# Kernel optimization log

Measured on AMD Instinct MI355X. Metric: run time of the kernel, lower is better.

The kernel has to match this reference:

```python
import jax, jax.numpy as jnp
import numpy as np

WINDOW_SIZE = 128  # matches init_kwargs


def setup_inputs() -> dict:
    key = jax.random.key(0)
    kq, kk, kv = jax.random.split(key, 3)
    B, H, S, D = 1, 8, 2048, 64
    q = jax.random.normal(kq, (B, H, S, D), dtype=jnp.float32)
    k = jax.random.normal(kk, (B, H, S, D), dtype=jnp.float32)
    v = jax.random.normal(kv, (B, H, S, D), dtype=jnp.float32)
    return {"q": q, "k": k, "v": v}


def reference(q, k, v):
    # q, k, v: [B, H, S, D]
    B, H, S, D = q.shape
    w = WINDOW_SIZE // 2  # half-window = 64
    offs = jnp.arange(-w, w + 1)                      # [W] with W = 2w+1 = 129
    pos = jnp.arange(S)[:, None] + offs[None, :]      # [S, W] absolute key index per query
    valid = (pos >= 0) & (pos < S)                    # edge clipping: start=max(0,i-w), end=min(S,i+w+1)
    pos_c = jnp.clip(pos, 0, S - 1)

    # Gather banded keys/values: [B, H, S, W, D]
    k_win = k[:, :, pos_c, :]
    v_win = v[:, :, pos_c, :]

    scale = 1.0 / jnp.sqrt(jnp.asarray(D, dtype=q.dtype))
    scores = jnp.einsum('bhsd,bhswd->bhsw', q, k_win) * scale  # [B, H, S, W]
    neg_inf = jnp.asarray(-jnp.inf, dtype=scores.dtype)
    scores = jnp.where(valid[None, None, :, :], scores, neg_inf)

    attn = jax.nn.softmax(scores, axis=-1)            # every row has >= w+1 valid entries, no NaNs
    out = jnp.einsum('bhsw,bhswd->bhsd', attn, v_win) # [B, H, S, D]
    return out
```

## Files before the change

kernel.cpp:

```cpp
#include <hip/hip_runtime.h>
#include <hip/hip_fp16.h>


#define SEQ 2048
#define NH 8
#define QB 64
#define ROWS 192
#define KSTR 72
#define PSTR 40

typedef _Float16 f16x8 __attribute__((ext_vector_type(8)));
typedef float    f32x4 __attribute__((ext_vector_type(4)));

static __device__ __forceinline__ ushort4 pack4(float4 f, float s) {
    union { _Float16 h[4]; ushort4 u; } p;
    p.h[0] = (_Float16)(f.x * s);
    p.h[1] = (_Float16)(f.y * s);
    p.h[2] = (_Float16)(f.z * s);
    p.h[3] = (_Float16)(f.w * s);
    return p.u;
}

__global__ __launch_bounds__(512) void local_attn(
    const float* __restrict__ q,
    const float* __restrict__ k,
    const float* __restrict__ v,
    float* __restrict__ out)
{
    __shared__ __align__(16) _Float16      Kl[ROWS * KSTR];
    __shared__ __align__(16) unsigned char VtB[64 * 384];
    __shared__ __align__(16) _Float16      Pm[8][16 * PSTR];
    __shared__ __align__(16) float         Cmb[4][64][20];

    const int tid  = threadIdx.x;
    const int lane = tid & 63;
    const int w    = tid >> 6;
    const int t    = w & 3;
    const int half = w >> 2;
    const int l15  = lane & 15;
    const int l4   = lane >> 4;
    const int bx   = blockIdx.x;
    const int h     = bx & 7;
    const int qbase = (bx >> 3) * QB;

    const float* kh = k + (size_t)h * SEQ * 64;
    const float* vh = v + (size_t)h * SEQ * 64;
    const float* qh = q + (size_t)h * SEQ * 64;

    const float* qrow = qh + (size_t)(qbase + t * 16 + l15) * 64 + l4 * 8;
    float4 q0 = *(const float4*)(qrow);
    float4 q1 = *(const float4*)(qrow + 4);
    float4 q2 = *(const float4*)(qrow + 32);
    float4 q3 = *(const float4*)(qrow + 36);
    union uf { f16x8 v; _Float16 hh[8]; };
    uf A0, A1;
    A0.hh[0] = (_Float16)(q0.x * 0.125f); A0.hh[1] = (_Float16)(q0.y * 0.125f);
    A0.hh[2] = (_Float16)(q0.z * 0.125f); A0.hh[3] = (_Float16)(q0.w * 0.125f);
    A0.hh[4] = (_Float16)(q1.x * 0.125f); A0.hh[5] = (_Float16)(q1.y * 0.125f);
    A0.hh[6] = (_Float16)(q1.z * 0.125f); A0.hh[7] = (_Float16)(q1.w * 0.125f);
    A1.hh[0] = (_Float16)(q2.x * 0.125f); A1.hh[1] = (_Float16)(q2.y * 0.125f);
    A1.hh[2] = (_Float16)(q2.z * 0.125f); A1.hh[3] = (_Float16)(q2.w * 0.125f);
    A1.hh[4] = (_Float16)(q3.x * 0.125f); A1.hh[5] = (_Float16)(q3.y * 0.125f);
    A1.hh[6] = (_Float16)(q3.z * 0.125f); A1.hh[7] = (_Float16)(q3.w * 0.125f);

    {
        const int d4  = (tid & 15) << 2;
        const int lr0 = tid >> 4;
        #pragma unroll
        for (int it = 0; it < 6; ++it) {
            const int lr = lr0 + it * 32;
            const int g  = qbase - 64 + lr;
            float4 kv4 = make_float4(0.f, 0.f, 0.f, 0.f);
            float4 vv4 = make_float4(0.f, 0.f, 0.f, 0.f);
            if (g >= 0 && g < SEQ) {
                kv4 = *(const float4*)(kh + (size_t)g * 64 + d4);
                vv4 = *(const float4*)(vh + (size_t)g * 64 + d4);
            }
            *(ushort4*)&Kl[lr * KSTR + d4] = pack4(kv4, 1.0f);
            float vs[4] = {vv4.x, vv4.y, vv4.z, vv4.w};
            #pragma unroll
            for (int i2 = 0; i2 < 4; ++i2) {
                int d = d4 + i2;
                int u = (lr >> 3) ^ (d & 7);
                *(_Float16*)&VtB[d * 384 + (u << 4) + (lr & 7) * 2] = (_Float16)vs[i2];
            }
        }
    }
    __syncthreads();

    _Float16* Pw = Pm[w];
    float rsum[4] = {0.f, 0.f, 0.f, 0.f};
    f32x4 o[4];
    #pragma unroll
    for (int dt = 0; dt < 4; ++dt) o[dt] = (f32x4){0.f, 0.f, 0.f, 0.f};

    #pragma unroll
    for (int c = 0; c < 3; ++c) {
        const int r0 = (half * 3 + c) * 32;

        #pragma unroll
        for (int t2 = 0; t2 < 2; ++t2) {
            const int r = r0 + t2 * 16 + l15;
            f16x8 b0 = *(const f16x8*)&Kl[r * KSTR + l4 * 8];
            f16x8 b1 = *(const f16x8*)&Kl[r * KSTR + 32 + l4 * 8];
            f32x4 cacc = {0.f, 0.f, 0.f, 0.f};
            cacc = __builtin_amdgcn_mfma_f32_16x16x32_f16(A0.v, b0, cacc, 0, 0, 0);
            cacc = __builtin_amdgcn_mfma_f32_16x16x32_f16(A1.v, b1, cacc, 0, 0, 0);
            const int g  = qbase - 64 + r;
            const bool gv = (g >= 0) & (g < SEQ);
            #pragma unroll
            for (int j = 0; j < 4; ++j) {
                const int qg = qbase + t * 16 + l4 * 4 + j;
                const bool valid = gv && (g >= qg - 64) && (g <= qg + 64);
                const float e = valid ? __expf(cacc[j]) : 0.f;
                rsum[j] += e;
                Pw[(l4 * 4 + j) * PSTR + t2 * 16 + l15] = (_Float16)e;
            }
        }

        asm volatile("s_waitcnt lgkmcnt(0)" ::: "memory");

        f16x8 a = *(const f16x8*)&Pw[l15 * PSTR + l4 * 8];
        #pragma unroll
        for (int dt = 0; dt < 4; ++dt) {
            const int dim = dt * 16 + l15;
            const int u   = ((r0 + l4 * 8) >> 3) ^ (dim & 7);
            f16x8 bb = *(const f16x8*)&VtB[dim * 384 + (u << 4)];
            o[dt] = __builtin_amdgcn_mfma_f32_16x16x32_f16(a, bb, o[dt], 0, 0, 0);
        }
    }

    if (half == 1) {
        #pragma unroll
        for (int dt = 0; dt < 4; ++dt)
            *(f32x4*)&Cmb[t][lane][dt * 4] = o[dt];
        f32x4 pr = {rsum[0], rsum[1], rsum[2], rsum[3]};
        *(f32x4*)&Cmb[t][lane][16] = pr;
    }
    __syncthreads();
    if (half == 0) {
        #pragma unroll
        for (int dt = 0; dt < 4; ++dt) {
            f32x4 p = *(const f32x4*)&Cmb[t][lane][dt * 4];
            o[dt] += p;
        }
        f32x4 pr = *(const f32x4*)&Cmb[t][lane][16];

        #pragma unroll
        for (int j = 0; j < 4; ++j) {
            float l = rsum[j] + pr[j];
            l += __shfl_xor(l, 1, 64);
            l += __shfl_xor(l, 2, 64);
            l += __shfl_xor(l, 4, 64);
            l += __shfl_xor(l, 8, 64);
            const float inv = 1.0f / l;
            const int qg = qbase + t * 16 + l4 * 4 + j;
            #pragma unroll
            for (int dt = 0; dt < 4; ++dt)
                out[((size_t)h * SEQ + qg) * 64 + dt * 16 + l15] = o[dt][j] * inv;
        }
    }
}

extern "C" void kernel_launch(void* const* d_in, const int* in_sizes, int n_in,
                              void* d_out, int out_size, void* d_ws, size_t ws_size,
                              hipStream_t stream)
{
    const float* q = (const float*)d_in[0];
    const float* k = (const float*)d_in[1];
    const float* v = (const float*)d_in[2];
    float* out = (float*)d_out;

    local_attn<<<256, 512, 0, stream>>>(q, k, v, out);
}
```

Measured before the change: 11.81 us.

## Halve query tile to 32 rows and run 512 blocks of 256 threads

Shrinks each block to 32 queries with a 160-row key/value band and four waves instead of eight. This launches twice as many blocks, so all CUs get work and each block has a shorter prologue. The score/PV chunk loop becomes an explicit 3-versus-2 chunk split between the two wave halves. In exchange, more K/V rows are reloaded per query and the two halves carry uneven work.

```diff
diff --git a/kernel.cpp b/kernel.cpp
--- a/kernel.cpp
+++ b/kernel.cpp
@@ -4,8 +4,8 @@
 
 #define SEQ 2048
 #define NH 8
-#define QB 64
-#define ROWS 192
+#define QB 32
+#define ROWS 160
 #define KSTR 72
 #define PSTR 40
 
@@ -21,7 +21,7 @@
     return p.u;
 }
 
-__global__ __launch_bounds__(512) void local_attn(
+__global__ __launch_bounds__(256, 2) void local_attn(
     const float* __restrict__ q,
     const float* __restrict__ k,
     const float* __restrict__ v,
@@ -29,14 +29,14 @@
 {
     __shared__ __align__(16) _Float16      Kl[ROWS * KSTR];
     __shared__ __align__(16) unsigned char VtB[64 * 384];
-    __shared__ __align__(16) _Float16      Pm[8][16 * PSTR];
-    __shared__ __align__(16) float         Cmb[4][64][20];
+    __shared__ __align__(16) _Float16      Pm[4][16 * PSTR];
+    __shared__ __align__(16) float         Cmb[2][64][20];
 
     const int tid  = threadIdx.x;
     const int lane = tid & 63;
     const int w    = tid >> 6;
-    const int t    = w & 3;
-    const int half = w >> 2;
+    const int t    = w & 1;
+    const int half = w >> 1;
     const int l15  = lane & 15;
     const int l4   = lane >> 4;
     const int bx   = blockIdx.x;
@@ -67,8 +67,8 @@
         const int d4  = (tid & 15) << 2;
         const int lr0 = tid >> 4;
         #pragma unroll
-        for (int it = 0; it < 6; ++it) {
-            const int lr = lr0 + it * 32;
+        for (int it = 0; it < 10; ++it) {
+            const int lr = lr0 + it * 16;
             const int g  = qbase - 64 + lr;
             float4 kv4 = make_float4(0.f, 0.f, 0.f, 0.f);
             float4 vv4 = make_float4(0.f, 0.f, 0.f, 0.f);
@@ -94,41 +94,48 @@
     #pragma unroll
     for (int dt = 0; dt < 4; ++dt) o[dt] = (f32x4){0.f, 0.f, 0.f, 0.f};
 
-    #pragma unroll
-    for (int c = 0; c < 3; ++c) {
-        const int r0 = (half * 3 + c) * 32;
+#define DO_CHUNK(R0)                                                          \
+    {                                                                         \
+        const int r0 = (R0);                                                  \
+        _Pragma("unroll")                                                     \
+        for (int t2 = 0; t2 < 2; ++t2) {                                      \
+            const int r = r0 + t2 * 16 + l15;                                 \
+            f16x8 b0 = *(const f16x8*)&Kl[r * KSTR + l4 * 8];                 \
+            f16x8 b1 = *(const f16x8*)&Kl[r * KSTR + 32 + l4 * 8];            \
+            f32x4 cacc = {0.f, 0.f, 0.f, 0.f};                                \
+            cacc = __builtin_amdgcn_mfma_f32_16x16x32_f16(A0.v, b0, cacc, 0, 0, 0); \
+            cacc = __builtin_amdgcn_mfma_f32_16x16x32_f16(A1.v, b1, cacc, 0, 0, 0); \
+            const int g  = qbase - 64 + r;                                    \
+            const bool gv = (g >= 0) & (g < SEQ);                             \
+            _Pragma("unroll")                                                 \
+            for (int j = 0; j < 4; ++j) {                                     \
+                const int qg = qbase + t * 16 + l4 * 4 + j;                   \
+                const bool valid = gv && (g >= qg - 64) && (g <= qg + 64);    \
+                const float e = valid ? __expf(cacc[j]) : 0.f;                \
+                rsum[j] += e;                                                 \
+                Pw[(l4 * 4 + j) * PSTR + t2 * 16 + l15] = (_Float16)e;        \
+            }                                                                 \
+        }                                                                     \
+        asm volatile("s_waitcnt lgkmcnt(0)" ::: "memory");                    \
+        f16x8 a = *(const f16x8*)&Pw[l15 * PSTR + l4 * 8];                    \
+        _Pragma("unroll")                                                     \
+        for (int dt = 0; dt < 4; ++dt) {                                      \
+            const int dim = dt * 16 + l15;                                    \
+            const int u   = ((r0 + l4 * 8) >> 3) ^ (dim & 7);                 \
+            f16x8 bb = *(const f16x8*)&VtB[dim * 384 + (u << 4)];             \
+            o[dt] = __builtin_amdgcn_mfma_f32_16x16x32_f16(a, bb, o[dt], 0, 0, 0); \
+        }                                                                     \
+    }
 
-        #pragma unroll
-        for (int t2 = 0; t2 < 2; ++t2) {
-            const int r = r0 + t2 * 16 + l15;
-            f16x8 b0 = *(const f16x8*)&Kl[r * KSTR + l4 * 8];
-            f16x8 b1 = *(const f16x8*)&Kl[r * KSTR + 32 + l4 * 8];
-            f32x4 cacc = {0.f, 0.f, 0.f, 0.f};
-            cacc = __builtin_amdgcn_mfma_f32_16x16x32_f16(A0.v, b0, cacc, 0, 0, 0);
-            cacc = __builtin_amdgcn_mfma_f32_16x16x32_f16(A1.v, b1, cacc, 0, 0, 0);
-            const int g  = qbase - 64 + r;
-            const bool gv = (g >= 0) & (g < SEQ);
-            #pragma unroll
-            for (int j = 0; j < 4; ++j) {
-                const int qg = qbase + t * 16 + l4 * 4 + j;
-                const bool valid = gv && (g >= qg - 64) && (g <= qg + 64);
-                const float e = valid ? __expf(cacc[j]) : 0.f;
-                rsum[j] += e;
-                Pw[(l4 * 4 + j) * PSTR + t2 * 16 + l15] = (_Float16)e;
-            }
-        }
-
-        asm volatile("s_waitcnt lgkmcnt(0)" ::: "memory");
-
-        f16x8 a = *(const f16x8*)&Pw[l15 * PSTR + l4 * 8];
-        #pragma unroll
-        for (int dt = 0; dt < 4; ++dt) {
-            const int dim = dt * 16 + l15;
-            const int u   = ((r0 + l4 * 8) >> 3) ^ (dim & 7);
-            f16x8 bb = *(const f16x8*)&VtB[dim * 384 + (u << 4)];
-            o[dt] = __builtin_amdgcn_mfma_f32_16x16x32_f16(a, bb, o[dt], 0, 0, 0);
-        }
+    if (half == 0) {
+        DO_CHUNK(0)
+        DO_CHUNK(32)
+        DO_CHUNK(64)
+    } else {
+        DO_CHUNK(96)
+        DO_CHUNK(128)
     }
+#undef DO_CHUNK
 
     if (half == 1) {
         #pragma unroll
@@ -171,5 +178,5 @@
     const float* v = (const float*)d_in[2];
     float* out = (float*)d_out;
 
-    local_attn<<<256, 512, 0, stream>>>(q, k, v, out);
+    local_attn<<<512, 256, 0, stream>>>(q, k, v, out);
 }
```

Result: slower. 12.79 us (+8.3%).

## Pre-convert K/V to swizzled fp16 workspace and load via global_load_lds

Applied to the files above, without the earlier changes.

Adds a separate pre-pass kernel that converts K and V to fp16 once into a padded, XOR-swizzled workspace, with V stored transposed. The attention kernel then copies its K/V tiles directly into LDS using global_load_lds DMA instead of per-thread float loads, conversion and scattered transposed stores. This removes the repeated conversion of overlapping windows and the bank-conflicted V transpose in the main kernel. In exchange it adds a second kernel launch and an extra workspace write and read, and it falls back to the old kernel when the workspace is too small.

```diff
diff --git a/kernel.cpp b/kernel.cpp
--- a/kernel.cpp
+++ b/kernel.cpp
@@ -6,28 +6,210 @@
 #define NH 8
 #define QB 64
 #define ROWS 192
-#define KSTR 72
 #define PSTR 40
+
+#define KHEAD 278528
+#define VOFF  2228224
+#define VROW  4352
+#define WSNEED (VOFF + 8 * 278528)
 
 typedef _Float16 f16x8 __attribute__((ext_vector_type(8)));
 typedef float    f32x4 __attribute__((ext_vector_type(4)));
 
-static __device__ __forceinline__ ushort4 pack4(float4 f, float s) {
-    union { _Float16 h[4]; ushort4 u; } p;
-    p.h[0] = (_Float16)(f.x * s);
-    p.h[1] = (_Float16)(f.y * s);
-    p.h[2] = (_Float16)(f.z * s);
-    p.h[3] = (_Float16)(f.w * s);
-    return p.u;
+#define GLOAD_LDS16(gsrc, ldst)                                              \
+    __builtin_amdgcn_global_load_lds(                                        \
+        (const __attribute__((address_space(1))) unsigned int*)(gsrc),       \
+        (__attribute__((address_space(3))) unsigned int*)(ldst), 16, 0, 0)
+
+__global__ __launch_bounds__(256) void convert_kv(
+    const float* __restrict__ k,
+    const float* __restrict__ v,
+    unsigned char* __restrict__ ws)
+{
+    const int b   = blockIdx.x;
+    const int tid = threadIdx.x;
+    if (b < 544) {
+        const int h      = b & 7;
+        const int rowblk = b >> 3;
+        const int gg     = rowblk * 32 + (tid >> 3);
+        const int c      = tid & 7;
+        const int g      = gg - 64;
+        union { _Float16 h8[8]; uint4 u; } pk;
+        if (g >= 0 && g < SEQ) {
+            const float* kr = k + ((size_t)h * SEQ + g) * 64 + c * 8;
+            float4 a = *(const float4*)kr;
+            float4 bb = *(const float4*)(kr + 4);
+            pk.h8[0] = (_Float16)a.x;  pk.h8[1] = (_Float16)a.y;
+            pk.h8[2] = (_Float16)a.z;  pk.h8[3] = (_Float16)a.w;
+            pk.h8[4] = (_Float16)bb.x; pk.h8[5] = (_Float16)bb.y;
+            pk.h8[6] = (_Float16)bb.z; pk.h8[7] = (_Float16)bb.w;
+        } else {
+            pk.u = make_uint4(0, 0, 0, 0);
+        }
+        *(uint4*)(ws + (size_t)h * KHEAD + (size_t)gg * 128
+                     + ((c ^ (gg & 7)) << 4)) = pk.u;
+    } else {
+        const int b2  = b - 544;
+        const int h   = b2 & 7;
+        const int grp = b2 >> 3;
+        const int d   = tid & 63;
+        const int gg0 = grp * 16 + (tid >> 6) * 4;
+        const int g0  = gg0 - 64;
+        union { _Float16 h4[4]; uint2 u; } pv;
+        #pragma unroll
+        for (int i = 0; i < 4; ++i) {
+            const int g = g0 + i;
+            const float val = (g >= 0 && g < SEQ)
+                ? v[((size_t)h * SEQ + g) * 64 + d] : 0.f;
+            pv.h4[i] = (_Float16)val;
+        }
+        const int chunk = (gg0 >> 3) ^ (d & 7);
+        *(uint2*)(ws + VOFF + (size_t)h * KHEAD + (size_t)d * VROW
+                     + (size_t)chunk * 16 + (gg0 & 7) * 2) = pv.u;
+    }
 }
 
-__global__ __launch_bounds__(512) void local_attn(
+__global__ __launch_bounds__(512) void local_attn_main(
+    const float* __restrict__ q,
+    const unsigned char* __restrict__ ws,
+    float* __restrict__ out)
+{
+    __shared__ __align__(16) _Float16      Kl[ROWS * 64];
+    __shared__ __align__(16) unsigned char VtB[64 * 384];
+    __shared__ __align__(16) _Float16      Pm[8][16 * PSTR];
+    __shared__ __align__(16) float         Cmb[4][64][20];
+
+    const int tid  = threadIdx.x;
+    const int lane = tid & 63;
+    const int w    = tid >> 6;
+    const int t    = w & 3;
+    const int half = w >> 2;
+    const int l15  = lane & 15;
+    const int l4   = lane >> 4;
+    const int bx   = blockIdx.x;
+    const int h     = bx & 7;
+    const int qbase = (bx >> 3) * QB;
+
+    const float* qh = q + (size_t)h * SEQ * 64;
+
+    const float* qrow = qh + (size_t)(qbase + t * 16 + l15) * 64 + l4 * 8;
+    float4 q0 = *(const float4*)(qrow);
+    float4 q1 = *(const float4*)(qrow + 4);
+    float4 q2 = *(const float4*)(qrow + 32);
+    float4 q3 = *(const float4*)(qrow + 36);
+
+    {
+        const unsigned char* kws = ws + (size_t)h * KHEAD + (size_t)qbase * 128;
+        const unsigned char* vws = ws + VOFF + (size_t)h * KHEAD;
+        const int vseg = qbase * 2;
+        #pragma unroll
+        for (int j = 0; j < 3; ++j) {
+            const int off = (w + j * 8) * 1024;
+            GLOAD_LDS16(kws + off + lane * 16, ((unsigned char*)Kl) + off);
+            const unsigned x = off + lane * 16;
+            const unsigned n = x >> 4;
+            const unsigned d = n / 24u;
+            const unsigned rb = (n - d * 24u) << 4;
+            GLOAD_LDS16(vws + (size_t)d * VROW + vseg + rb,
+                        ((unsigned char*)VtB) + off);
+        }
+    }
+
+    union uf { f16x8 v; _Float16 hh[8]; };
+    uf A0, A1;
+    A0.hh[0] = (_Float16)(q0.x * 0.125f); A0.hh[1] = (_Float16)(q0.y * 0.125f);
+    A0.hh[2] = (_Float16)(q0.z * 0.125f); A0.hh[3] = (_Float16)(q0.w * 0.125f);
+    A0.hh[4] = (_Float16)(q1.x * 0.125f); A0.hh[5] = (_Float16)(q1.y * 0.125f);
+    A0.hh[6] = (_Float16)(q1.z * 0.125f); A0.hh[7] = (_Float16)(q1.w * 0.125f);
+    A1.hh[0] = (_Float16)(q2.x * 0.125f); A1.hh[1] = (_Float16)(q2.y * 0.125f);
+    A1.hh[2] = (_Float16)(q2.z * 0.125f); A1.hh[3] = (_Float16)(q2.w * 0.125f);
+    A1.hh[4] = (_Float16)(q3.x * 0.125f); A1.hh[5] = (_Float16)(q3.y * 0.125f);
+    A1.hh[6] = (_Float16)(q3.z * 0.125f); A1.hh[7] = (_Float16)(q3.w * 0.125f);
+
+    asm volatile("s_waitcnt vmcnt(0)" ::: "memory");
+    __syncthreads();
+
+    _Float16* Pw = Pm[w];
+    float rsum[4] = {0.f, 0.f, 0.f, 0.f};
+    f32x4 o[4];
+    #pragma unroll
+    for (int dt = 0; dt < 4; ++dt) o[dt] = (f32x4){0.f, 0.f, 0.f, 0.f};
+
+    #pragma unroll
+    for (int c = 0; c < 3; ++c) {
+        const int r0 = (half * 3 + c) * 32;
+
+        #pragma unroll
+        for (int t2 = 0; t2 < 2; ++t2) {
+            const int r = r0 + t2 * 16 + l15;
+            f16x8 b0 = *(const f16x8*)&Kl[r * 64 + (( l4      ^ (r & 7)) << 3)];
+            f16x8 b1 = *(const f16x8*)&Kl[r * 64 + (((l4 + 4) ^ (r & 7)) << 3)];
+            f32x4 cacc = {0.f, 0.f, 0.f, 0.f};
+            cacc = __builtin_amdgcn_mfma_f32_16x16x32_f16(A0.v, b0, cacc, 0, 0, 0);
+            cacc = __builtin_amdgcn_mfma_f32_16x16x32_f16(A1.v, b1, cacc, 0, 0, 0);
+            const int g  = qbase - 64 + r;
+            const bool gv = (g >= 0) & (g < SEQ);
+            #pragma unroll
+            for (int j = 0; j < 4; ++j) {
+                const int qg = qbase + t * 16 + l4 * 4 + j;
+                const bool valid = gv && (g >= qg - 64) && (g <= qg + 64);
+                const float e = valid ? __expf(cacc[j]) : 0.f;
+                rsum[j] += e;
+                Pw[(l4 * 4 + j) * PSTR + t2 * 16 + l15] = (_Float16)e;
+            }
+        }
+
+        asm volatile("s_waitcnt lgkmcnt(0)" ::: "memory");
+
+        f16x8 a = *(const f16x8*)&Pw[l15 * PSTR + l4 * 8];
+        #pragma unroll
+        for (int dt = 0; dt < 4; ++dt) {
+            const int dim = dt * 16 + l15;
+            const int u   = ((r0 + l4 * 8) >> 3) ^ (dim & 7);
+            f16x8 bb = *(const f16x8*)&VtB[dim * 384 + (u << 4)];
+            o[dt] = __builtin_amdgcn_mfma_f32_16x16x32_f16(a, bb, o[dt], 0, 0, 0);
+        }
+    }
+
+    if (half == 1) {
+        #pragma unroll
+        for (int dt = 0; dt < 4; ++dt)
+            *(f32x4*)&Cmb[t][lane][dt * 4] = o[dt];
+        f32x4 pr = {rsum[0], rsum[1], rsum[2], rsum[3]};
+        *(f32x4*)&Cmb[t][lane][16] = pr;
+    }
+    __syncthreads();
+    if (half == 0) {
+        #pragma unroll
+        for (int dt = 0; dt < 4; ++dt) {
+            f32x4 p = *(const f32x4*)&Cmb[t][lane][dt * 4];
+            o[dt] += p;
+        }
+        f32x4 pr = *(const f32x4*)&Cmb[t][lane][16];
+
+        #pragma unroll
+        for (int j = 0; j < 4; ++j) {
+            float l = rsum[j] + pr[j];
+            l += __shfl_xor(l, 1, 64);
+            l += __shfl_xor(l, 2, 64);
+            l += __shfl_xor(l, 4, 64);
+            l += __shfl_xor(l, 8, 64);
+            const float inv = 1.0f / l;
+            const int qg = qbase + t * 16 + l4 * 4 + j;
+            #pragma unroll
+            for (int dt = 0; dt < 4; ++dt)
+                out[((size_t)h * SEQ + qg) * 64 + dt * 16 + l15] = o[dt][j] * inv;
+        }
+    }
+}
+
+__global__ __launch_bounds__(512) void local_attn_fb(
     const float* __restrict__ q,
     const float* __restrict__ k,
     const float* __restrict__ v,
     float* __restrict__ out)
 {
-    __shared__ __align__(16) _Float16      Kl[ROWS * KSTR];
+    __shared__ __align__(16) _Float16      Kl[ROWS * 72];
     __shared__ __align__(16) unsigned char VtB[64 * 384];
     __shared__ __align__(16) _Float16      Pm[8][16 * PSTR];
     __shared__ __align__(16) float         Cmb[4][64][20];
@@ -76,7 +258,10 @@
                 kv4 = *(const float4*)(kh + (size_t)g * 64 + d4);
                 vv4 = *(const float4*)(vh + (size_t)g * 64 + d4);
             }
-            *(ushort4*)&Kl[lr * KSTR + d4] = pack4(kv4, 1.0f);
+            union { _Float16 hh[4]; ushort4 u; } pk;
+            pk.hh[0] = (_Float16)kv4.x; pk.hh[1] = (_Float16)kv4.y;
+            pk.hh[2] = (_Float16)kv4.z; pk.hh[3] = (_Float16)kv4.w;
+            *(ushort4*)&Kl[lr * 72 + d4] = pk.u;
             float vs[4] = {vv4.x, vv4.y, vv4.z, vv4.w};
             #pragma unroll
             for (int i2 = 0; i2 < 4; ++i2) {
@@ -97,12 +282,11 @@
     #pragma unroll
     for (int c = 0; c < 3; ++c) {
         const int r0 = (half * 3 + c) * 32;
-
         #pragma unroll
         for (int t2 = 0; t2 < 2; ++t2) {
             const int r = r0 + t2 * 16 + l15;
-            f16x8 b0 = *(const f16x8*)&Kl[r * KSTR + l4 * 8];
-            f16x8 b1 = *(const f16x8*)&Kl[r * KSTR + 32 + l4 * 8];
+            f16x8 b0 = *(const f16x8*)&Kl[r * 72 + l4 * 8];
+            f16x8 b1 = *(const f16x8*)&Kl[r * 72 + 32 + l4 * 8];
             f32x4 cacc = {0.f, 0.f, 0.f, 0.f};
             cacc = __builtin_amdgcn_mfma_f32_16x16x32_f16(A0.v, b0, cacc, 0, 0, 0);
             cacc = __builtin_amdgcn_mfma_f32_16x16x32_f16(A1.v, b1, cacc, 0, 0, 0);
@@ -117,9 +301,7 @@
                 Pw[(l4 * 4 + j) * PSTR + t2 * 16 + l15] = (_Float16)e;
             }
         }
-
         asm volatile("s_waitcnt lgkmcnt(0)" ::: "memory");
-
         f16x8 a = *(const f16x8*)&Pw[l15 * PSTR + l4 * 8];
         #pragma unroll
         for (int dt = 0; dt < 4; ++dt) {
@@ -145,7 +327,6 @@
             o[dt] += p;
         }
         f32x4 pr = *(const f32x4*)&Cmb[t][lane][16];
-
         #pragma unroll
         for (int j = 0; j < 4; ++j) {
             float l = rsum[j] + pr[j];
@@ -171,5 +352,10 @@
     const float* v = (const float*)d_in[2];
     float* out = (float*)d_out;
 
-    local_attn<<<256, 512, 0, stream>>>(q, k, v, out);
+    if (ws_size >= (size_t)WSNEED) {
+        convert_kv<<<1632, 256, 0, stream>>>(k, v, (unsigned char*)d_ws);
+        local_attn_main<<<256, 512, 0, stream>>>(q, (const unsigned char*)d_ws, out);
+    } else {
+        local_attn_fb<<<256, 512, 0, stream>>>(q, k, v, out);
+    }
 }
```

After: 15.63 us. +32.3%, slower.

## Stage K/V via global_load_lds into swizzled fp32 LDS tiles

Applied to the files above, without the earlier changes.

Replaces register-staged K/V loads with direct global-to-LDS async loads (global_load_lds, 16 bytes) into XOR-swizzled fp32 buffers, clamping out-of-range rows instead of zero-filling. K stays in fp32 in LDS and is converted to fp16 per MFMA operand, while V is transposed from the LDS copy into the existing swizzled fp16 layout. This aims to cut VGPR traffic and overlap the Q conversion with the loads, but it raises LDS use to about 150 KB per block, adds an extra barrier and transpose pass, and doubles K read bytes from LDS.

```diff
diff --git a/kernel.cpp b/kernel.cpp
--- a/kernel.cpp
+++ b/kernel.cpp
@@ -3,23 +3,17 @@
 
 
 #define SEQ 2048
-#define NH 8
 #define QB 64
 #define ROWS 192
-#define KSTR 72
 #define PSTR 40
 
 typedef _Float16 f16x8 __attribute__((ext_vector_type(8)));
 typedef float    f32x4 __attribute__((ext_vector_type(4)));
 
-static __device__ __forceinline__ ushort4 pack4(float4 f, float s) {
-    union { _Float16 h[4]; ushort4 u; } p;
-    p.h[0] = (_Float16)(f.x * s);
-    p.h[1] = (_Float16)(f.y * s);
-    p.h[2] = (_Float16)(f.z * s);
-    p.h[3] = (_Float16)(f.w * s);
-    return p.u;
-}
+#define GLOAD_LDS16(gsrc, ldst)                                              \
+    __builtin_amdgcn_global_load_lds(                                        \
+        (const __attribute__((address_space(1))) unsigned int*)(gsrc),       \
+        (__attribute__((address_space(3))) unsigned int*)(ldst), 16, 0, 0)
 
 __global__ __launch_bounds__(512) void local_attn(
     const float* __restrict__ q,
@@ -27,10 +21,12 @@
     const float* __restrict__ v,
     float* __restrict__ out)
 {
-    __shared__ __align__(16) _Float16      Kl[ROWS * KSTR];
-    __shared__ __align__(16) unsigned char VtB[64 * 384];
-    __shared__ __align__(16) _Float16      Pm[8][16 * PSTR];
-    __shared__ __align__(16) float         Cmb[4][64][20];
+    __shared__ __align__(16) unsigned char LDS[153600];
+    unsigned char* KF   = LDS;
+    unsigned char* VF   = LDS + 49152;
+    unsigned char* VtB  = LDS + 98304;
+    _Float16*      PmB  = (_Float16*)(LDS + 122880);
+    float*         CmbB = (float*)(LDS + 133120);
 
     const int tid  = threadIdx.x;
     const int lane = tid & 63;
@@ -43,15 +39,29 @@
     const int h     = bx & 7;
     const int qbase = (bx >> 3) * QB;
 
+    const float* qh = q + (size_t)h * SEQ * 64;
     const float* kh = k + (size_t)h * SEQ * 64;
     const float* vh = v + (size_t)h * SEQ * 64;
-    const float* qh = q + (size_t)h * SEQ * 64;
 
     const float* qrow = qh + (size_t)(qbase + t * 16 + l15) * 64 + l4 * 8;
     float4 q0 = *(const float4*)(qrow);
     float4 q1 = *(const float4*)(qrow + 4);
     float4 q2 = *(const float4*)(qrow + 32);
     float4 q3 = *(const float4*)(qrow + 36);
+
+    #pragma unroll
+    for (int j = 0; j < 6; ++j) {
+        const int s    = tid + j * 512;
+        const int row  = s >> 4;
+        const int cpos = s & 15;
+        const int gch  = cpos ^ ((row & 7) << 1);
+        int g = qbase - 64 + row;
+        g = g < 0 ? 0 : (g > SEQ - 1 ? SEQ - 1 : g);
+        const size_t goff = (size_t)g * 64 + gch * 4;
+        GLOAD_LDS16(kh + goff, KF + s * 16);
+        GLOAD_LDS16(vh + goff, VF + s * 16);
+    }
+
     union uf { f16x8 v; _Float16 hh[8]; };
     uf A0, A1;
     A0.hh[0] = (_Float16)(q0.x * 0.125f); A0.hh[1] = (_Float16)(q0.y * 0.125f);
@@ -63,32 +73,29 @@
     A1.hh[4] = (_Float16)(q3.x * 0.125f); A1.hh[5] = (_Float16)(q3.y * 0.125f);
     A1.hh[6] = (_Float16)(q3.z * 0.125f); A1.hh[7] = (_Float16)(q3.w * 0.125f);
 
+    asm volatile("s_waitcnt vmcnt(0)" ::: "memory");
+    __syncthreads();
+
     {
-        const int d4  = (tid & 15) << 2;
-        const int lr0 = tid >> 4;
+        const int d0 = (tid & 15) * 4;
+        const int rr = (tid >> 4) * 6;
         #pragma unroll
-        for (int it = 0; it < 6; ++it) {
-            const int lr = lr0 + it * 32;
-            const int g  = qbase - 64 + lr;
-            float4 kv4 = make_float4(0.f, 0.f, 0.f, 0.f);
-            float4 vv4 = make_float4(0.f, 0.f, 0.f, 0.f);
-            if (g >= 0 && g < SEQ) {
-                kv4 = *(const float4*)(kh + (size_t)g * 64 + d4);
-                vv4 = *(const float4*)(vh + (size_t)g * 64 + d4);
-            }
-            *(ushort4*)&Kl[lr * KSTR + d4] = pack4(kv4, 1.0f);
-            float vs[4] = {vv4.x, vv4.y, vv4.z, vv4.w};
+        for (int i = 0; i < 6; ++i) {
+            const int r    = rr + i;
+            const int cpos = (tid & 15) ^ ((r & 7) << 1);
+            f32x4 tmp = *(const f32x4*)(VF + r * 256 + cpos * 16);
             #pragma unroll
             for (int i2 = 0; i2 < 4; ++i2) {
-                int d = d4 + i2;
-                int u = (lr >> 3) ^ (d & 7);
-                *(_Float16*)&VtB[d * 384 + (u << 4) + (lr & 7) * 2] = (_Float16)vs[i2];
+                const int d = d0 + i2;
+                const int u = (r >> 3) ^ (d & 7);
+                *(_Float16*)&VtB[d * 384 + (u << 4) + (r & 7) * 2] =
+                    (_Float16)tmp[i2];
             }
         }
     }
     __syncthreads();
 
-    _Float16* Pw = Pm[w];
+    _Float16* Pw = PmB + w * 16 * PSTR;
     float rsum[4] = {0.f, 0.f, 0.f, 0.f};
     f32x4 o[4];
     #pragma unroll
@@ -101,11 +108,24 @@
         #pragma unroll
         for (int t2 = 0; t2 < 2; ++t2) {
             const int r = r0 + t2 * 16 + l15;
-            f16x8 b0 = *(const f16x8*)&Kl[r * KSTR + l4 * 8];
-            f16x8 b1 = *(const f16x8*)&Kl[r * KSTR + 32 + l4 * 8];
+            const int x = (r & 7) << 1;
+            const unsigned a0 = r * 256 + ((unsigned)((l4 * 2) ^ x) << 4);
+            const unsigned a1 = r * 256 + ((unsigned)((l4 * 2 + 8) ^ x) << 4);
+            f32x4 k0 = *(const f32x4*)(KF + a0);
+            f32x4 k1 = *(const f32x4*)(KF + a0 + 16);
+            f32x4 k2 = *(const f32x4*)(KF + a1);
+            f32x4 k3 = *(const f32x4*)(KF + a1 + 16);
+            uf b0, b1;
+            #pragma unroll
+            for (int j = 0; j < 4; ++j) {
+                b0.hh[j]     = (_Float16)k0[j];
+                b0.hh[j + 4] = (_Float16)k1[j];
+                b1.hh[j]     = (_Float16)k2[j];
+                b1.hh[j + 4] = (_Float16)k3[j];
+            }
             f32x4 cacc = {0.f, 0.f, 0.f, 0.f};
-            cacc = __builtin_amdgcn_mfma_f32_16x16x32_f16(A0.v, b0, cacc, 0, 0, 0);
-            cacc = __builtin_amdgcn_mfma_f32_16x16x32_f16(A1.v, b1, cacc, 0, 0, 0);
+            cacc = __builtin_amdgcn_mfma_f32_16x16x32_f16(A0.v, b0.v, cacc, 0, 0, 0);
+            cacc = __builtin_amdgcn_mfma_f32_16x16x32_f16(A1.v, b1.v, cacc, 0, 0, 0);
             const int g  = qbase - 64 + r;
             const bool gv = (g >= 0) & (g < SEQ);
             #pragma unroll
@@ -130,21 +150,22 @@
         }
     }
 
+    float* Cl = CmbB + (t * 64 + lane) * 20;
     if (half == 1) {
         #pragma unroll
         for (int dt = 0; dt < 4; ++dt)
-            *(f32x4*)&Cmb[t][lane][dt * 4] = o[dt];
+            *(f32x4*)(Cl + dt * 4) = o[dt];
         f32x4 pr = {rsum[0], rsum[1], rsum[2], rsum[3]};
-        *(f32x4*)&Cmb[t][lane][16] = pr;
+        *(f32x4*)(Cl + 16) = pr;
     }
     __syncthreads();
     if (half == 0) {
         #pragma unroll
         for (int dt = 0; dt < 4; ++dt) {
-            f32x4 p = *(const f32x4*)&Cmb[t][lane][dt * 4];
+            f32x4 p = *(const f32x4*)(Cl + dt * 4);
             o[dt] += p;
         }
-        f32x4 pr = *(const f32x4*)&Cmb[t][lane][16];
+        f32x4 pr = *(const f32x4*)(Cl + 16);
 
         #pragma unroll
         for (int j = 0; j < 4; ++j) {
```

Result: slower. 12.65 us (+7.1%).
